# Performance work log

Measured on AMD Instinct MI355X. Metric: run time of the kernel, lower is better.

The kernel has to match this reference:

```python
import jax, jax.numpy as jnp
import numpy as np
from jax import lax

B, S, D, E, K, MULT = 4, 2048, 1024, 1536, 4, 4
LN_EPS = 1e-5

def log_g(x):
    return jnp.where(x >= 0, jnp.log(jax.nn.relu(x) + 0.5), -jax.nn.softplus(-x))

def layer_norm(x, g, b):
    mu = jnp.mean(x, axis=-1, keepdims=True)
    var = jnp.mean((x - mu) ** 2, axis=-1, keepdims=True)
    return (x - mu) * lax.rsqrt(var + LN_EPS) * g + b

def setup_inputs() -> dict:
    key = jax.random.key(0)
    ks = jax.random.split(key, 16)
    s = lambda fan: 1.0 / np.sqrt(fan)
    inp = {
        'x': jax.random.normal(ks[0], (B, S, D), dtype=jnp.float32),
        'conv_dw_w': jax.random.uniform(ks[1], (D, 1, K), jnp.float32, -s(K), s(K)),
        'conv_dw_b': jax.random.uniform(ks[2], (D,), jnp.float32, -s(K), s(K)),
        'conv_pw_w': jax.random.uniform(ks[3], (D, D), jnp.float32, -s(D), s(D)),
        'conv_pw_b': jax.random.uniform(ks[4], (D,), jnp.float32, -s(D), s(D)),
        'ln1_g': jnp.ones((D,), jnp.float32),
        'ln1_b': jnp.zeros((D,), jnp.float32),
        'w_f': jax.random.uniform(ks[5], (E, D), jnp.float32, -s(D), s(D)),
        'w_i': jax.random.uniform(ks[6], (E, D), jnp.float32, -s(D), s(D)),
        'w_h': jax.random.uniform(ks[7], (E, D), jnp.float32, -s(D), s(D)),
        'w_down': jax.random.uniform(ks[8], (D, E), jnp.float32, -s(E), s(E)),
        'ln2_g': jnp.ones((D,), jnp.float32),
        'ln2_b': jnp.zeros((D,), jnp.float32),
        'mlp_w1': jax.random.uniform(ks[9], (MULT * D, D), jnp.float32, -s(D), s(D)),
        'mlp_b1': jax.random.uniform(ks[10], (MULT * D,), jnp.float32, -s(D), s(D)),
        'mlp_w2': jax.random.uniform(ks[11], (D, MULT * D), jnp.float32, -s(MULT * D), s(MULT * D)),
        'mlp_b2': jax.random.uniform(ks[12], (D,), jnp.float32, -s(MULT * D), s(MULT * D)),
    }
    return inp

def _forward(x, conv_dw_w, conv_dw_b, conv_pw_w, conv_pw_b, ln1_g, ln1_b,
             w_f, w_i, w_h, w_down, ln2_g, ln2_b, mlp_w1, mlp_b1, mlp_w2, mlp_b2):
    residual = x
    # causal depthwise conv + pointwise conv (channels-first over time)
    xc = jnp.transpose(x, (0, 2, 1))                       # (B, D, S)
    xc = jnp.pad(xc, ((0, 0), (0, 0), (K - 1, 0)))         # left causal pad
    dw = lax.conv_general_dilated(xc, conv_dw_w, (1,), 'VALID',
                                  feature_group_count=D,
                                  dimension_numbers=('NCH', 'OIH', 'NCH'))
    dw = dw + conv_dw_b[None, :, None]
    pw = jnp.einsum('bds,ed->bes', dw, conv_pw_w) + conv_pw_b[None, :, None]
    x = jnp.transpose(pw, (0, 2, 1)) + residual
    x = layer_norm(x, ln1_g, ln1_b)
    # minLSTM log-space parallel scan
    log_f = -jax.nn.softplus(-(x @ w_f.T))                 # (B, S, E)
    log_i = -jax.nn.softplus(-(x @ w_i.T))
    log_th = log_g(x @ w_h.T)
    log_h0 = jnp.full((B, 1, E), jnp.log(jnp.float32(0.5)), dtype=x.dtype)
    log_values = jnp.concatenate([log_h0, log_i + log_th], axis=1)   # (B, S+1, E)
    a_star = jnp.pad(jnp.cumsum(log_f, axis=1), ((0, 0), (1, 0), (0, 0)))
    log_h = a_star + lax.cumlogsumexp(log_values - a_star, axis=1)
    h = jnp.exp(log_h)[:, 1:]                              # (B, S, E)
    x = h @ w_down.T + residual
    x = layer_norm(x, ln2_g, ln2_b)
    # MLP (exact GELU like torch default); dropout with p=0 is identity
    hmid = jax.nn.gelu(x @ mlp_w1.T + mlp_b1, approximate=False)
    return hmid @ mlp_w2.T + mlp_b2

def reference(x, conv_dw_w, conv_dw_b, conv_pw_w, conv_pw_b, ln1_g, ln1_b,
              w_f, w_i, w_h, w_down, ln2_g, ln2_b, mlp_w1, mlp_b1, mlp_w2, mlp_b2):
    return _forward(x, conv_dw_w, conv_dw_b, conv_pw_w, conv_pw_b, ln1_g, ln1_b,
                    w_f, w_i, w_h, w_down, ln2_g, ln2_b, mlp_w1, mlp_b1, mlp_w2, mlp_b2)
```

## Files before the change

### kernel.cpp

```cpp
#include <hip/hip_runtime.h>
#include <hip/hip_bf16.h>
#include <math.h>

using bf16 = __hip_bfloat16;
typedef __attribute__((ext_vector_type(8))) short s8v;
typedef __attribute__((ext_vector_type(4))) float f32x4;

#define B_  4
#define S_  2048
#define D_  1024
#define E_  1536
#define M_  (B_*S_)
#define BE_ (B_*E_)
#define NCH 16
#define CHS (S_/NCH)

__device__ __forceinline__ float b2f(bf16 h) { return __bfloat162float(h); }
__device__ __forceinline__ bf16  f2b(float f) { return __float2bfloat16(f); }

struct __align__(8)  bh4 { bf16 h[4]; };

__device__ __forceinline__ void gld16(const void* g, void* l) {
  __builtin_amdgcn_global_load_lds((const __attribute__((address_space(1))) void*)g,
                                   (__attribute__((address_space(3))) void*)l, 16, 0, 0);
}

__global__ __launch_bounds__(256) void cvt_k(const float* __restrict__ s,
                                             bf16* __restrict__ d, int n)
{
  int i = (blockIdx.x * 256 + threadIdx.x) * 4;
  if (i < n) {
    float4 v = *(const float4*)(s + i);
    bh4 o;
    o.h[0] = f2b(v.x); o.h[1] = f2b(v.y); o.h[2] = f2b(v.z); o.h[3] = f2b(v.w);
    *(bh4*)(d + i) = o;
  }
}

__global__ __launch_bounds__(256) void dwconv_k(const float* __restrict__ x,
                                                const float* __restrict__ w,
                                                const float* __restrict__ bias,
                                                bf16* __restrict__ out)
{
  int m = blockIdx.x;
  int s = m & (S_ - 1);
  int d = threadIdx.x * 4;
  float wf[4][4];
#pragma unroll
  for (int i = 0; i < 4; ++i) {
    float4 wr = *(const float4*)(w + (d + i) * 4);
    wf[i][0] = wr.x; wf[i][1] = wr.y; wf[i][2] = wr.z; wf[i][3] = wr.w;
  }
  float4 bb = *(const float4*)(bias + d);
  float acc[4] = {bb.x, bb.y, bb.z, bb.w};
#pragma unroll
  for (int k = 0; k < 4; ++k) {
    if (s - 3 + k >= 0) {
      float4 xv = *(const float4*)(x + (size_t)(m - 3 + k) * D_ + d);
      acc[0] += xv.x * wf[0][k];
      acc[1] += xv.y * wf[1][k];
      acc[2] += xv.z * wf[2][k];
      acc[3] += xv.w * wf[3][k];
    }
  }
  bh4 ov;
#pragma unroll
  for (int i = 0; i < 4; ++i) ov.h[i] = f2b(acc[i]);
  *(bh4*)(out + (size_t)m * D_ + d) = ov;
}

template<int EPI>
__global__ __launch_bounds__(256) void gemm_ab(const bf16* __restrict__ A, int lda,
                                               const bf16* __restrict__ Bb, int ldb,
                                               const float* __restrict__ bias,
                                               const float* __restrict__ resid,
                                               bf16* outH, bf16* outH2, float* outF,
                                               int M, int N, int K)
{
  __shared__ __align__(16) bf16 lsA[128 * 64];
  __shared__ __align__(16) bf16 lsB[128 * 64];
  const int tid  = threadIdx.x;
  const int lane = tid & 63;
  const int wave = tid >> 6;
  const int m0 = blockIdx.y * 128, n0 = blockIdx.x * 128;
  const int wm = (wave >> 1) * 64, wn = (wave & 1) * 64;
  const int r = lane & 15, q = lane >> 4;
  const int sw = r & 7;
  f32x4 acc[4][4] = {};

  for (int k0 = 0; k0 < K; k0 += 64) {
#pragma unroll
    for (int i = 0; i < 4; ++i) {
      int c = i * 256 + tid;
      int row = c >> 3, cc = (c & 7) ^ (row & 7);
      gld16(A  + (size_t)(m0 + row) * lda + k0 + cc * 8, (char*)lsA + c * 16);
      gld16(Bb + (size_t)(n0 + row) * ldb + k0 + cc * 8, (char*)lsB + c * 16);
    }
    __syncthreads();
#pragma unroll
    for (int kk = 0; kk < 64; kk += 32) {
      const int j = (kk >> 3) + q;
      s8v af[4], bfr[4];
#pragma unroll
      for (int t = 0; t < 4; ++t) {
        af[t]  = *(const s8v*)((char*)lsA + (((wm + t * 16 + r) << 3) + (j ^ sw)) * 16);
        bfr[t] = *(const s8v*)((char*)lsB + (((wn + t * 16 + r) << 3) + (j ^ sw)) * 16);
      }
#pragma unroll
      for (int mi = 0; mi < 4; ++mi)
#pragma unroll
        for (int ni = 0; ni < 4; ++ni)
          acc[mi][ni] = __builtin_amdgcn_mfma_f32_16x16x32_bf16(af[mi], bfr[ni], acc[mi][ni], 0, 0, 0);
    }
    __syncthreads();
  }

#pragma unroll
  for (int mi = 0; mi < 4; ++mi) {
#pragma unroll
    for (int j = 0; j < 4; ++j) {
      int row = m0 + wm + mi * 16 + q * 4 + j;
#pragma unroll
      for (int ni = 0; ni < 4; ++ni) {
        int col = n0 + wn + ni * 16 + r;
        size_t idx = (size_t)row * N + col;
        float v = acc[mi][ni][j];
        if constexpr (EPI == 0) {
          outH[idx] = f2b(v + bias[col] + resid[idx]);
        } else if constexpr (EPI == 1) {
          if (col < 1536) outH [(size_t)row * 1536 + col]        = f2b(v);
          else            outH2[(size_t)row * 1536 + col - 1536] = f2b(v);
        } else if constexpr (EPI == 2) {
          float gh = (v >= 0.f) ? (v + 0.5f) : (1.f / (1.f + expf(-v)));
          float iv = 1.f / (1.f + expf(-b2f(outH[idx])));
          outH[idx] = f2b(gh * iv);
        } else if constexpr (EPI == 3) {
          outH[idx] = f2b(v + resid[idx]);
        } else if constexpr (EPI == 4) {
          float u = v + bias[col];
          outH[idx] = f2b(0.5f * u * (1.f + erff(u * 0.70710678118f)));
        } else {
          outF[idx] = v + bias[col];
        }
      }
    }
  }
}

__global__ __launch_bounds__(256) void ln_k(const bf16* __restrict__ y,
                                            const float* __restrict__ g,
                                            const float* __restrict__ b,
                                            bf16* __restrict__ out)
{
  __shared__ float sm[8];
  int row = blockIdx.x;
  bh4 v4 = ((const bh4*)(y + (size_t)row * D_))[threadIdx.x];
  float v0 = b2f(v4.h[0]), v1 = b2f(v4.h[1]), v2 = b2f(v4.h[2]), v3 = b2f(v4.h[3]);
  float s = v0 + v1 + v2 + v3;
#pragma unroll
  for (int o = 32; o; o >>= 1) s += __shfl_down(s, o);
  int lane = threadIdx.x & 63, w = threadIdx.x >> 6;
  if (lane == 0) sm[w] = s;
  __syncthreads();
  float mu = (sm[0] + sm[1] + sm[2] + sm[3]) * (1.f / D_);
  float d0 = v0 - mu, d1 = v1 - mu, d2 = v2 - mu, d3 = v3 - mu;
  float qq = d0 * d0 + d1 * d1 + d2 * d2 + d3 * d3;
#pragma unroll
  for (int o = 32; o; o >>= 1) qq += __shfl_down(qq, o);
  if (lane == 0) sm[4 + w] = qq;
  __syncthreads();
  float var = (sm[4] + sm[5] + sm[6] + sm[7]) * (1.f / D_);
  float inv = rsqrtf(var + 1e-5f);
  int c = threadIdx.x * 4;
  float4 gv = *(const float4*)(g + c);
  float4 bv = *(const float4*)(b + c);
  bh4 ov;
  ov.h[0] = f2b(d0 * inv * gv.x + bv.x);
  ov.h[1] = f2b(d1 * inv * gv.y + bv.y);
  ov.h[2] = f2b(d2 * inv * gv.z + bv.z);
  ov.h[3] = f2b(d3 * inv * gv.w + bv.w);
  *(bh4*)(out + (size_t)row * D_ + c) = ov;
}

__global__ __launch_bounds__(256) void scanA2_k(const bf16* __restrict__ fpre,
                                                const bf16* __restrict__ g,
                                                float* __restrict__ Fc, float* __restrict__ Gc)
{
  int gth = blockIdx.x * 256 + threadIdx.x;
  int c = gth / BE_, be = gth % BE_;
  int b = be / E_,  e = be % E_;
  size_t idx = (size_t)b * S_ * E_ + (size_t)c * CHS * E_ + e;
  float F = 1.f, G = 0.f;
  for (int sl = 0; sl < CHS; ++sl, idx += E_) {
    float fv = 1.f / (1.f + expf(-b2f(fpre[idx])));
    F *= fv;
    G = fv * G + b2f(g[idx]);
  }
  Fc[gth] = F; Gc[gth] = G;
}

__global__ __launch_bounds__(256) void scanB_k(const float* __restrict__ Fc,
                                               const float* __restrict__ Gc,
                                               float* __restrict__ hst)
{
  int be = blockIdx.x * 256 + threadIdx.x;
  float h = 0.5f;
#pragma unroll
  for (int c = 0; c < NCH; ++c) {
    hst[c * BE_ + be] = h;
    h = Fc[c * BE_ + be] * h + Gc[c * BE_ + be];
  }
}

__global__ __launch_bounds__(256) void scanC2_k(const bf16* __restrict__ fpre,
                                                bf16* g,
                                                const float* __restrict__ hst)
{
  int gth = blockIdx.x * 256 + threadIdx.x;
  int c = gth / BE_, be = gth % BE_;
  int b = be / E_,  e = be % E_;
  size_t idx = (size_t)b * S_ * E_ + (size_t)c * CHS * E_ + e;
  float h = hst[gth];
  for (int sl = 0; sl < CHS; ++sl, idx += E_) {
    float fv = 1.f / (1.f + expf(-b2f(fpre[idx])));
    h = fv * h + b2f(g[idx]);
    g[idx] = f2b(h);
  }
}

extern "C" void kernel_launch(void* const* d_in, const int* in_sizes, int n_in,
                              void* d_out, int out_size, void* d_ws, size_t ws_size,
                              hipStream_t stream)
{
  (void)in_sizes; (void)n_in; (void)out_size; (void)ws_size;
  const float* x      = (const float*)d_in[0];
  const float* cdw_w  = (const float*)d_in[1];
  const float* cdw_b  = (const float*)d_in[2];
  const float* cpw_w  = (const float*)d_in[3];
  const float* cpw_b  = (const float*)d_in[4];
  const float* ln1_g  = (const float*)d_in[5];
  const float* ln1_b  = (const float*)d_in[6];
  const float* w_f    = (const float*)d_in[7];
  const float* w_i    = (const float*)d_in[8];
  const float* w_h    = (const float*)d_in[9];
  const float* w_down = (const float*)d_in[10];
  const float* ln2_g  = (const float*)d_in[11];
  const float* ln2_b  = (const float*)d_in[12];
  const float* mlp_w1 = (const float*)d_in[13];
  const float* mlp_b1 = (const float*)d_in[14];
  const float* mlp_w2 = (const float*)d_in[15];
  const float* mlp_b2 = (const float*)d_in[16];
  char* ws = (char*)d_ws;
  float* outF = (float*)d_out;

  bf16* dw_buf = (bf16*)(ws + 0);
  bf16* xln    = (bf16*)(ws + 0);
  float* Fc    = (float*)(ws + 0);
  float* Gc    = (float*)(ws + 393216);
  float* hst   = (float*)(ws + 786432);
  bf16* yb     = (bf16*)(ws + 16777216);
  bf16* hmid   = (bf16*)(ws + 16777216);
  bf16* fpre   = (bf16*)(ws + 33554432);
  bf16* gvals  = (bf16*)(ws + 58720256);
  bf16* pwb    = (bf16*)(ws + 83886080);
  bf16* wfib   = (bf16*)(ws + 85983232);
  bf16* whb    = (bf16*)(ws + 92274688);
  bf16* wdb    = (bf16*)(ws + 95420416);
  bf16* w1b    = (bf16*)(ws + 98566144);
  bf16* w2b    = (bf16*)(ws + 106954752);

  cvt_k<<<(D_*D_)/1024,   256, 0, stream>>>(cpw_w,  pwb, D_*D_);
  cvt_k<<<(E_*D_)/1024,   256, 0, stream>>>(w_f,    wfib, E_*D_);
  cvt_k<<<(E_*D_)/1024,   256, 0, stream>>>(w_i,    wfib + E_*D_, E_*D_);
  cvt_k<<<(E_*D_)/1024,   256, 0, stream>>>(w_h,    whb, E_*D_);
  cvt_k<<<(D_*E_)/1024,   256, 0, stream>>>(w_down, wdb, D_*E_);
  cvt_k<<<(4*D_*D_)/1024, 256, 0, stream>>>(mlp_w1, w1b, 4*D_*D_);
  cvt_k<<<(4*D_*D_)/1024, 256, 0, stream>>>(mlp_w2, w2b, 4*D_*D_);

  dwconv_k<<<M_, 256, 0, stream>>>(x, cdw_w, cdw_b, dw_buf);
  gemm_ab<0><<<dim3(8, 64), 256, 0, stream>>>(dw_buf, D_, pwb, D_, cpw_b, x, yb, nullptr, nullptr, M_, D_, D_);
  ln_k<<<M_, 256, 0, stream>>>(yb, ln1_g, ln1_b, xln);
  gemm_ab<1><<<dim3(24, 64), 256, 0, stream>>>(xln, D_, wfib, D_, nullptr, nullptr, fpre, gvals, nullptr, M_, 3072, D_);
  gemm_ab<2><<<dim3(12, 64), 256, 0, stream>>>(xln, D_, whb, D_, nullptr, nullptr, gvals, nullptr, nullptr, M_, E_, D_);
  scanA2_k<<<(BE_*NCH)/256, 256, 0, stream>>>(fpre, gvals, Fc, Gc);
  scanB_k<<<BE_/256, 256, 0, stream>>>(Fc, Gc, hst);
  scanC2_k<<<(BE_*NCH)/256, 256, 0, stream>>>(fpre, gvals, hst);
  gemm_ab<3><<<dim3(8, 64), 256, 0, stream>>>(gvals, E_, wdb, E_, nullptr, x, yb, nullptr, nullptr, M_, D_, E_);
  ln_k<<<M_, 256, 0, stream>>>(yb, ln2_g, ln2_b, xln);
  gemm_ab<4><<<dim3(32, 64), 256, 0, stream>>>(xln, D_, w1b, D_, mlp_b1, nullptr, hmid, nullptr, nullptr, M_, 4*D_, D_);
  gemm_ab<5><<<dim3(8, 64), 256, 0, stream>>>(hmid, 4*D_, w2b, 4*D_, mlp_b2, nullptr, nullptr, nullptr, outF, M_, D_, 4*D_);
}
```

Before: 658.1 us.

## Vectorize chunked scan, tile depthwise conv, and merge weight conversions into one kernel

```diff
diff --git a/kernel.cpp b/kernel.cpp
--- a/kernel.cpp
+++ b/kernel.cpp
@@ -12,29 +12,52 @@
 #define E_  1536
 #define M_  (B_*S_)
 #define BE_ (B_*E_)
-#define NCH 16
+#define NCH 128
 #define CHS (S_/NCH)
+#define TS_ 16
 
 __device__ __forceinline__ float b2f(bf16 h) { return __bfloat162float(h); }
 __device__ __forceinline__ bf16  f2b(float f) { return __float2bfloat16(f); }
+__device__ __forceinline__ float su2f(short v) {
+  unsigned u = ((unsigned)(unsigned short)v) << 16;
+  return __builtin_bit_cast(float, u);
+}
+__device__ __forceinline__ short f2bs(float f) { return __builtin_bit_cast(short, f2b(f)); }
 
 struct __align__(8)  bh4 { bf16 h[4]; };
+struct __align__(16) bh8 { bf16 h[8]; };
 
 __device__ __forceinline__ void gld16(const void* g, void* l) {
   __builtin_amdgcn_global_load_lds((const __attribute__((address_space(1))) void*)g,
                                    (__attribute__((address_space(3))) void*)l, 16, 0, 0);
 }
 
-__global__ __launch_bounds__(256) void cvt_k(const float* __restrict__ s,
-                                             bf16* __restrict__ d, int n)
-{
-  int i = (blockIdx.x * 256 + threadIdx.x) * 4;
-  if (i < n) {
-    float4 v = *(const float4*)(s + i);
-    bh4 o;
-    o.h[0] = f2b(v.x); o.h[1] = f2b(v.y); o.h[2] = f2b(v.z); o.h[3] = f2b(v.w);
-    *(bh4*)(d + i) = o;
-  }
+__global__ __launch_bounds__(256) void cvt7_k(const float* __restrict__ s0,
+                                              const float* __restrict__ s1,
+                                              const float* __restrict__ s2,
+                                              const float* __restrict__ s3,
+                                              const float* __restrict__ s4,
+                                              const float* __restrict__ s5,
+                                              const float* __restrict__ s6,
+                                              bf16* __restrict__ d)
+{
+  size_t i = ((size_t)blockIdx.x * 256 + threadIdx.x) * 4;
+  const float* s; size_t off;
+  if (i < 4194304) {
+    if (i < 1048576)      { s = s0; off = 0; }
+    else if (i < 2621440) { s = s1; off = 1048576; }
+    else                  { s = s2; off = 2621440; }
+  } else if (i < 7340032) {
+    if (i < 5767168)      { s = s3; off = 4194304; }
+    else                  { s = s4; off = 5767168; }
+  } else {
+    if (i < 11534336)     { s = s5; off = 7340032; }
+    else                  { s = s6; off = 11534336; }
+  }
+  float4 v = *(const float4*)(s + (i - off));
+  bh4 o;
+  o.h[0] = f2b(v.x); o.h[1] = f2b(v.y); o.h[2] = f2b(v.z); o.h[3] = f2b(v.w);
+  *(bh4*)(d + i) = o;
 }
 
 __global__ __launch_bounds__(256) void dwconv_k(const float* __restrict__ x,
@@ -42,8 +65,8 @@
                                                 const float* __restrict__ bias,
                                                 bf16* __restrict__ out)
 {
-  int m = blockIdx.x;
-  int s = m & (S_ - 1);
+  int m0 = blockIdx.x * TS_;
+  int s0 = m0 & (S_ - 1);
   int d = threadIdx.x * 4;
   float wf[4][4];
 #pragma unroll
@@ -52,21 +75,55 @@
     wf[i][0] = wr.x; wf[i][1] = wr.y; wf[i][2] = wr.z; wf[i][3] = wr.w;
   }
   float4 bb = *(const float4*)(bias + d);
-  float acc[4] = {bb.x, bb.y, bb.z, bb.w};
-#pragma unroll
-  for (int k = 0; k < 4; ++k) {
-    if (s - 3 + k >= 0) {
-      float4 xv = *(const float4*)(x + (size_t)(m - 3 + k) * D_ + d);
-      acc[0] += xv.x * wf[0][k];
-      acc[1] += xv.y * wf[1][k];
-      acc[2] += xv.z * wf[2][k];
-      acc[3] += xv.w * wf[3][k];
-    }
-  }
-  bh4 ov;
-#pragma unroll
-  for (int i = 0; i < 4; ++i) ov.h[i] = f2b(acc[i]);
-  *(bh4*)(out + (size_t)m * D_ + d) = ov;
+
+  float4 xr[TS_ + 3];
+#pragma unroll
+  for (int j = 0; j < TS_ + 3; ++j) {
+    int srow = s0 - 3 + j;
+    if (srow >= 0) xr[j] = *(const float4*)(x + (size_t)(m0 - 3 + j) * D_ + d);
+    else           xr[j] = make_float4(0.f, 0.f, 0.f, 0.f);
+  }
+#pragma unroll
+  for (int t = 0; t < TS_; ++t) {
+    float a0 = bb.x, a1 = bb.y, a2 = bb.z, a3 = bb.w;
+#pragma unroll
+    for (int k = 0; k < 4; ++k) {
+      float4 xv = xr[t + k];
+      a0 += xv.x * wf[0][k];
+      a1 += xv.y * wf[1][k];
+      a2 += xv.z * wf[2][k];
+      a3 += xv.w * wf[3][k];
+    }
+    bh4 ov;
+    ov.h[0] = f2b(a0); ov.h[1] = f2b(a1); ov.h[2] = f2b(a2); ov.h[3] = f2b(a3);
+    *(bh4*)(out + (size_t)(m0 + t) * D_ + d) = ov;
+  }
+}
+
+template<int EPI>
+__device__ __forceinline__ void epi_store(float v, int row, int col, int N,
+                                          const float* __restrict__ bias,
+                                          const float* __restrict__ resid,
+                                          bf16* outH, bf16* outH2, float* outF)
+{
+  size_t idx = (size_t)row * N + col;
+  if constexpr (EPI == 0) {
+    outH[idx] = f2b(v + bias[col] + resid[idx]);
+  } else if constexpr (EPI == 1) {
+    if (col < 1536) outH [(size_t)row * 1536 + col]        = f2b(v);
+    else            outH2[(size_t)row * 1536 + col - 1536] = f2b(v);
+  } else if constexpr (EPI == 2) {
+    float gh = (v >= 0.f) ? (v + 0.5f) : (1.f / (1.f + expf(-v)));
+    float iv = 1.f / (1.f + expf(-b2f(outH[idx])));
+    outH[idx] = f2b(gh * iv);
+  } else if constexpr (EPI == 3) {
+    outH[idx] = f2b(v + resid[idx]);
+  } else if constexpr (EPI == 4) {
+    float u = v + bias[col];
+    outH[idx] = f2b(0.5f * u * (1.f + erff(u * 0.70710678118f)));
+  } else {
+    outF[idx] = v + bias[col];
+  }
 }
 
 template<int EPI>
@@ -116,35 +173,14 @@
   }
 
 #pragma unroll
-  for (int mi = 0; mi < 4; ++mi) {
+  for (int mi = 0; mi < 4; ++mi)
 #pragma unroll
     for (int j = 0; j < 4; ++j) {
       int row = m0 + wm + mi * 16 + q * 4 + j;
 #pragma unroll
-      for (int ni = 0; ni < 4; ++ni) {
-        int col = n0 + wn + ni * 16 + r;
-        size_t idx = (size_t)row * N + col;
-        float v = acc[mi][ni][j];
-        if constexpr (EPI == 0) {
-          outH[idx] = f2b(v + bias[col] + resid[idx]);
-        } else if constexpr (EPI == 1) {
-          if (col < 1536) outH [(size_t)row * 1536 + col]        = f2b(v);
-          else            outH2[(size_t)row * 1536 + col - 1536] = f2b(v);
-        } else if constexpr (EPI == 2) {
-          float gh = (v >= 0.f) ? (v + 0.5f) : (1.f / (1.f + expf(-v)));
-          float iv = 1.f / (1.f + expf(-b2f(outH[idx])));
-          outH[idx] = f2b(gh * iv);
-        } else if constexpr (EPI == 3) {
-          outH[idx] = f2b(v + resid[idx]);
-        } else if constexpr (EPI == 4) {
-          float u = v + bias[col];
-          outH[idx] = f2b(0.5f * u * (1.f + erff(u * 0.70710678118f)));
-        } else {
-          outF[idx] = v + bias[col];
-        }
-      }
-    }
-  }
+      for (int ni = 0; ni < 4; ++ni)
+        epi_store<EPI>(acc[mi][ni][j], row, n0 + wn + ni * 16 + r, N, bias, resid, outH, outH2, outF);
+    }
 }
 
 __global__ __launch_bounds__(256) void ln_k(const bf16* __restrict__ y,
@@ -186,17 +222,30 @@
                                                 const bf16* __restrict__ g,
                                                 float* __restrict__ Fc, float* __restrict__ Gc)
 {
-  int gth = blockIdx.x * 256 + threadIdx.x;
-  int c = gth / BE_, be = gth % BE_;
-  int b = be / E_,  e = be % E_;
+  int t = blockIdx.x * 256 + threadIdx.x;
+  int c = t / (BE_ / 8);
+  int col = t % (BE_ / 8);
+  int be8 = col * 8;
+  int b = be8 / E_, e = be8 % E_;
   size_t idx = (size_t)b * S_ * E_ + (size_t)c * CHS * E_ + e;
-  float F = 1.f, G = 0.f;
+  float F[8], G[8];
+#pragma unroll
+  for (int j = 0; j < 8; ++j) { F[j] = 1.f; G[j] = 0.f; }
   for (int sl = 0; sl < CHS; ++sl, idx += E_) {
-    float fv = 1.f / (1.f + expf(-b2f(fpre[idx])));
-    F *= fv;
-    G = fv * G + b2f(g[idx]);
-  }
-  Fc[gth] = F; Gc[gth] = G;
+    s8v fv8 = *(const s8v*)(fpre + idx);
+    s8v gv8 = *(const s8v*)(g + idx);
+#pragma unroll
+    for (int j = 0; j < 8; ++j) {
+      float fv = 1.f / (1.f + expf(-su2f(fv8[j])));
+      F[j] *= fv;
+      G[j] = fv * G[j] + su2f(gv8[j]);
+    }
+  }
+  size_t o = (size_t)c * BE_ + be8;
+  *(float4*)(Fc + o)     = make_float4(F[0], F[1], F[2], F[3]);
+  *(float4*)(Fc + o + 4) = make_float4(F[4], F[5], F[6], F[7]);
+  *(float4*)(Gc + o)     = make_float4(G[0], G[1], G[2], G[3]);
+  *(float4*)(Gc + o + 4) = make_float4(G[4], G[5], G[6], G[7]);
 }
 
 __global__ __launch_bounds__(256) void scanB_k(const float* __restrict__ Fc,
@@ -205,7 +254,7 @@
 {
   int be = blockIdx.x * 256 + threadIdx.x;
   float h = 0.5f;
-#pragma unroll
+#pragma unroll 16
   for (int c = 0; c < NCH; ++c) {
     hst[c * BE_ + be] = h;
     h = Fc[c * BE_ + be] * h + Gc[c * BE_ + be];
@@ -216,15 +265,27 @@
                                                 bf16* g,
                                                 const float* __restrict__ hst)
 {
-  int gth = blockIdx.x * 256 + threadIdx.x;
-  int c = gth / BE_, be = gth % BE_;
-  int b = be / E_,  e = be % E_;
+  int t = blockIdx.x * 256 + threadIdx.x;
+  int c = t / (BE_ / 8);
+  int col = t % (BE_ / 8);
+  int be8 = col * 8;
+  int b = be8 / E_, e = be8 % E_;
   size_t idx = (size_t)b * S_ * E_ + (size_t)c * CHS * E_ + e;
-  float h = hst[gth];
+  size_t o = (size_t)c * BE_ + be8;
+  float4 h0 = *(const float4*)(hst + o);
+  float4 h1 = *(const float4*)(hst + o + 4);
+  float h[8] = {h0.x, h0.y, h0.z, h0.w, h1.x, h1.y, h1.z, h1.w};
   for (int sl = 0; sl < CHS; ++sl, idx += E_) {
-    float fv = 1.f / (1.f + expf(-b2f(fpre[idx])));
-    h = fv * h + b2f(g[idx]);
-    g[idx] = f2b(h);
+    s8v fv8 = *(const s8v*)(fpre + idx);
+    s8v gv8 = *(const s8v*)(g + idx);
+    bh8 ov;
+#pragma unroll
+    for (int j = 0; j < 8; ++j) {
+      float fv = 1.f / (1.f + expf(-su2f(fv8[j])));
+      h[j] = fv * h[j] + su2f(gv8[j]);
+      ov.h[j] = f2b(h[j]);
+    }
+    *(bh8*)(g + idx) = ov;
   }
 }
 
@@ -256,8 +317,8 @@
   bf16* dw_buf = (bf16*)(ws + 0);
   bf16* xln    = (bf16*)(ws + 0);
   float* Fc    = (float*)(ws + 0);
-  float* Gc    = (float*)(ws + 393216);
-  float* hst   = (float*)(ws + 786432);
+  float* Gc    = (float*)(ws + 3145728);
+  float* hst   = (float*)(ws + 6291456);
   bf16* yb     = (bf16*)(ws + 16777216);
   bf16* hmid   = (bf16*)(ws + 16777216);
   bf16* fpre   = (bf16*)(ws + 33554432);
@@ -269,22 +330,16 @@
   bf16* w1b    = (bf16*)(ws + 98566144);
   bf16* w2b    = (bf16*)(ws + 106954752);
 
-  cvt_k<<<(D_*D_)/1024,   256, 0, stream>>>(cpw_w,  pwb, D_*D_);
-  cvt_k<<<(E_*D_)/1024,   256, 0, stream>>>(w_f,    wfib, E_*D_);
-  cvt_k<<<(E_*D_)/1024,   256, 0, stream>>>(w_i,    wfib + E_*D_, E_*D_);
-  cvt_k<<<(E_*D_)/1024,   256, 0, stream>>>(w_h,    whb, E_*D_);
-  cvt_k<<<(D_*E_)/1024,   256, 0, stream>>>(w_down, wdb, D_*E_);
-  cvt_k<<<(4*D_*D_)/1024, 256, 0, stream>>>(mlp_w1, w1b, 4*D_*D_);
-  cvt_k<<<(4*D_*D_)/1024, 256, 0, stream>>>(mlp_w2, w2b, 4*D_*D_);
-
-  dwconv_k<<<M_, 256, 0, stream>>>(x, cdw_w, cdw_b, dw_buf);
+  cvt7_k<<<15360, 256, 0, stream>>>(cpw_w, w_f, w_i, w_h, w_down, mlp_w1, mlp_w2, pwb);
+
+  dwconv_k<<<M_/TS_, 256, 0, stream>>>(x, cdw_w, cdw_b, dw_buf);
   gemm_ab<0><<<dim3(8, 64), 256, 0, stream>>>(dw_buf, D_, pwb, D_, cpw_b, x, yb, nullptr, nullptr, M_, D_, D_);
   ln_k<<<M_, 256, 0, stream>>>(yb, ln1_g, ln1_b, xln);
   gemm_ab<1><<<dim3(24, 64), 256, 0, stream>>>(xln, D_, wfib, D_, nullptr, nullptr, fpre, gvals, nullptr, M_, 3072, D_);
   gemm_ab<2><<<dim3(12, 64), 256, 0, stream>>>(xln, D_, whb, D_, nullptr, nullptr, gvals, nullptr, nullptr, M_, E_, D_);
-  scanA2_k<<<(BE_*NCH)/256, 256, 0, stream>>>(fpre, gvals, Fc, Gc);
+  scanA2_k<<<(NCH*BE_/8)/256, 256, 0, stream>>>(fpre, gvals, Fc, Gc);
   scanB_k<<<BE_/256, 256, 0, stream>>>(Fc, Gc, hst);
-  scanC2_k<<<(BE_*NCH)/256, 256, 0, stream>>>(fpre, gvals, hst);
+  scanC2_k<<<(NCH*BE_/8)/256, 256, 0, stream>>>(fpre, gvals, hst);
   gemm_ab<3><<<dim3(8, 64), 256, 0, stream>>>(gvals, E_, wdb, E_, nullptr, x, yb, nullptr, nullptr, M_, D_, E_);
   ln_k<<<M_, 256, 0, stream>>>(yb, ln2_g, ln2_b, xln);
   gemm_ab<4><<<dim3(32, 64), 256, 0, stream>>>(xln, D_, w1b, D_, mlp_b1, nullptr, hmid, nullptr, nullptr, M_, 4*D_, D_);
```

Result: faster. 624.1 us (-5.2%).
